# Optimization experiments

Hardware: AMD Instinct MI355X
Metric: run time of the kernel (lower is better)

The kernel has to match this reference:

```python
import jax, jax.numpy as jnp
import numpy as np

LN_EPS = 1e-5

def setup_inputs() -> dict:
    key = jax.random.key(0)
    k1, k2, k3 = jax.random.split(key, 3)
    L, B, D = 2048, 8, 1024
    x = jax.random.normal(k1, (L, B, D), dtype=jnp.float32)
    c = jnp.zeros((B, D), dtype=jnp.float32)
    W = jax.random.normal(k2, (D, 3 * D), dtype=jnp.float32) * 0.02
    # bias init from _init_bias: u-bias 0, f-bias 0.5, r-bias 0
    b = jnp.concatenate([jnp.zeros(D), jnp.full((D,), 0.5), jnp.zeros(D)]).astype(jnp.float32)
    gamma = jnp.ones((D,), dtype=jnp.float32)
    beta = jnp.zeros((D,), dtype=jnp.float32)
    return {"x": x, "c": c, "W": W, "b": b, "gamma": gamma, "beta": beta}

def reference(x, c, W, b, gamma, beta):
    # LayerNorm over last dim
    mu = jnp.mean(x, axis=-1, keepdims=True)
    var = jnp.mean(jnp.square(x - mu), axis=-1, keepdims=True)
    x_norm = (x - mu) * jax.lax.rsqrt(var + LN_EPS) * gamma + beta
    # Fused u/f/r projection: [L,B,3D]
    ufr = jnp.einsum('lbd,de->lbe', x_norm, W) + b
    u, f, r = jnp.split(ufr, 3, axis=-1)
    f_gate = jax.nn.sigmoid(f)
    r_gate = jax.nn.sigmoid(r)
    # Linear recurrence c_t = f_t * c_{t-1} + (1-f_t) * u_t via scan over time
    def step(c_prev, fu):
        f_t, u_t = fu
        c_t = f_t * c_prev + (1.0 - f_t) * u_t
        return c_t, c_t
    last_c, c_stack = jax.lax.scan(step, c, (f_gate, u))
    hs = r_gate * jnp.tanh(c_stack) + (1.0 - r_gate) * x_norm
    return x + hs, last_c
```

## Files before the change

kernel.cpp:

```cpp
#include <hip/hip_runtime.h>
#include <hip/hip_bf16.h>


typedef unsigned short u16;
typedef __bf16 bf16x8 __attribute__((ext_vector_type(8)));
typedef float f32x4 __attribute__((ext_vector_type(4)));

#define L_DIM 2048
#define B_DIM 8
#define D_DIM 1024
#define M_DIM (L_DIM * B_DIM)
#define K_DIM D_DIM
#define N_DIM (3 * D_DIM)
#define NCH 32
#define CLEN (L_DIM / NCH)
#define NT (K_DIM / 64)

#define LDS_A 0
#define LDS_B 65536
#define LDS_DUMMY 131072
#define LDS_TOTAL 147456

__device__ __forceinline__ float bf2f(u16 h) {
    unsigned int u = ((unsigned int)h) << 16;
    float f;
    __builtin_memcpy(&f, &u, 4);
    return f;
}

__device__ __forceinline__ u16 f2bf(float f) {
    unsigned int u;
    __builtin_memcpy(&u, &f, 4);
    u = u + 0x7fff + ((u >> 16) & 1);
    return (u16)(u >> 16);
}

__device__ __forceinline__ void async16(void* lds, const void* g) {
    __builtin_amdgcn_global_load_lds(
        (const __attribute__((address_space(1))) void*)g,
        (__attribute__((address_space(3))) void*)lds, 16, 0, 0);
}

__global__ __launch_bounds__(256) void ln_kernel(const float* __restrict__ x,
                                                 const float* __restrict__ gamma,
                                                 const float* __restrict__ beta,
                                                 u16* __restrict__ xn) {
    int row = blockIdx.x;
    int tid = threadIdx.x;
    const float4* xr = (const float4*)(x + (size_t)row * D_DIM);
    float4 v = xr[tid];
    float s = v.x + v.y + v.z + v.w;
    float q = v.x * v.x + v.y * v.y + v.z * v.z + v.w * v.w;
    #pragma unroll
    for (int off = 32; off; off >>= 1) {
        s += __shfl_down(s, off);
        q += __shfl_down(q, off);
    }
    __shared__ float ss[4], qq[4];
    int lane = tid & 63, wv = tid >> 6;
    if (lane == 0) { ss[wv] = s; qq[wv] = q; }
    __syncthreads();
    s = ss[0] + ss[1] + ss[2] + ss[3];
    q = qq[0] + qq[1] + qq[2] + qq[3];
    float mu = s * (1.0f / D_DIM);
    float var = q * (1.0f / D_DIM) - mu * mu;
    float rs = rsqrtf(var + 1e-5f);
    float4 g = ((const float4*)gamma)[tid];
    float4 bt = ((const float4*)beta)[tid];
    ushort4 o;
    o.x = f2bf((v.x - mu) * rs * g.x + bt.x);
    o.y = f2bf((v.y - mu) * rs * g.y + bt.y);
    o.z = f2bf((v.z - mu) * rs * g.z + bt.z);
    o.w = f2bf((v.w - mu) * rs * g.w + bt.w);
    ((ushort4*)(xn + (size_t)row * D_DIM))[tid] = o;
}

__global__ __launch_bounds__(256) void wt_kernel(const float* __restrict__ W,
                                                 u16* __restrict__ Wt) {
    __shared__ float t[64][65];
    int k0 = blockIdx.x * 64;
    int n0 = blockIdx.y * 64;
    int col = threadIdx.x & 63;
    int rg4 = threadIdx.x >> 6;
    #pragma unroll
    for (int j = 0; j < 16; ++j) {
        int r = rg4 * 16 + j;
        t[r][col] = W[(size_t)(k0 + r) * N_DIM + n0 + col];
    }
    __syncthreads();
    #pragma unroll
    for (int j = 0; j < 16; ++j) {
        int nr = rg4 * 16 + j;
        Wt[(size_t)(n0 + nr) * K_DIM + k0 + col] = f2bf(t[col][nr]);
    }
}

__device__ __forceinline__ void stage_half(const u16* __restrict__ gsrc, int base0,
                                           int t, int h, char* lds, int ldsOp,
                                           int tid, int wave) {
    int tc = (t < NT) ? t : 0;
    int k0 = tc * 64;
    char* dst0 = (t < NT) ? (lds + ldsOp + (t & 1) * 32768 + h * 16384)
                          : (lds + LDS_DUMMY);
    #pragma unroll
    for (int s = 0; s < 2; ++s) {
        int c = s * 512 + tid;
        int row = h * 128 + (c >> 3);
        int cc = (c & 7) ^ (row & 7);
        async16(dst0 + s * 8192 + wave * 1024,
                gsrc + (size_t)(base0 + row) * K_DIM + k0 + cc * 8);
    }
}

__global__ __launch_bounds__(512, 2) void gemm_kernel(const u16* __restrict__ A,
                                                      const u16* __restrict__ Bt,
                                                      const float* __restrict__ bias,
                                                      u16* __restrict__ uo,
                                                      u16* __restrict__ fo,
                                                      u16* __restrict__ ro) {
    extern __shared__ char lds[];
    const int tid = threadIdx.x;
    const int wave = tid >> 6, lane = tid & 63;
    const int lm = lane & 15, lg = lane >> 4;
    const int wm = wave >> 2, wn = wave & 3;
    const int m0 = blockIdx.x * 256;
    const int n0 = blockIdx.y * 256;

    f32x4 acc[8][4] = {};
    bf16x8 av[4][2], aw[4][2], bv[4][2];

#define LDA(dst, bb, mf0)                                                       \
    do { _Pragma("unroll")                                                      \
        for (int q = 0; q < 4; ++q) {                                           \
            int row_ = wm * 128 + ((mf0) + q) * 16 + lm;                        \
            const char* p_ = lds + LDS_A + (bb) * 32768 + row_ * 128;           \
            _Pragma("unroll")                                                   \
            for (int kk = 0; kk < 2; ++kk)                                      \
                dst[q][kk] = *(const bf16x8*)(p_ + ((((kk << 2) | lg) ^ (row_ & 7)) << 4)); \
        } } while (0)

#define LDB(bb, kk)                                                             \
    do { _Pragma("unroll")                                                      \
        for (int nf = 0; nf < 4; ++nf) {                                        \
            int row_ = wn * 64 + nf * 16 + lm;                                  \
            bv[nf][kk] = *(const bf16x8*)(lds + LDS_B + (bb) * 32768 + row_ * 128 \
                                          + ((((kk << 2) | lg) ^ (row_ & 7)) << 4)); \
        } } while (0)

#define MFMA16(r0, afr, kk)                                                     \
    do { _Pragma("unroll")                                                      \
        for (int q = 0; q < 4; ++q)                                             \
            _Pragma("unroll")                                                   \
            for (int nf = 0; nf < 4; ++nf)                                      \
                acc[(r0) + q][nf] = __builtin_amdgcn_mfma_f32_16x16x32_bf16(    \
                    afr[q][kk], bv[nf][kk], acc[(r0) + q][nf], 0, 0, 0);        \
    } while (0)

#define PH_SYNC()                                                               \
    do { __builtin_amdgcn_s_barrier();                                          \
         asm volatile("s_waitcnt lgkmcnt(0)");                                  \
         __builtin_amdgcn_sched_barrier(0); } while (0)

#define TILE_BODY(t, bb, last)                                                  \
    do {                                                                        \
                 \
        LDA(av, bb, 0);                                                         \
        LDB(bb, 0);                                                             \
        stage_half(A, m0, (t) + 1, 0, lds, LDS_A, tid, wave);                   \
        PH_SYNC();                                                              \
        __builtin_amdgcn_s_setprio(1);                                          \
        MFMA16(0, av, 0);                                                       \
        __builtin_amdgcn_s_setprio(0);                                          \
        __builtin_amdgcn_s_barrier();                                           \
                                     \
        LDB(bb, 1);                                                             \
        stage_half(A, m0, (t) + 1, 1, lds, LDS_A, tid, wave);                   \
        PH_SYNC();                                                              \
        __builtin_amdgcn_s_setprio(1);                                          \
        MFMA16(0, av, 1);                                                       \
        __builtin_amdgcn_s_setprio(0);                                          \
        __builtin_amdgcn_s_barrier();                                           \
                                   \
        LDA(aw, bb, 4);                                                         \
        stage_half(Bt, n0, (t) + 2, 0, lds, LDS_B, tid, wave);                  \
        PH_SYNC();                                                              \
        __builtin_amdgcn_s_setprio(1);                                          \
        MFMA16(4, aw, 0);                                                       \
        __builtin_amdgcn_s_setprio(0);                                          \
        __builtin_amdgcn_s_barrier();                                           \
                         \
        stage_half(Bt, n0, (t) + 2, 1, lds, LDS_B, tid, wave);                  \
        __builtin_amdgcn_s_barrier();                                           \
        __builtin_amdgcn_s_setprio(1);                                          \
        MFMA16(4, aw, 1);                                                       \
        __builtin_amdgcn_s_setprio(0);                                          \
        if (!(last)) asm volatile("s_waitcnt vmcnt(4)" ::: "memory");           \
        __builtin_amdgcn_s_barrier();                                           \
    } while (0)

    stage_half(A, m0, 0, 0, lds, LDS_A, tid, wave);
    stage_half(A, m0, 0, 1, lds, LDS_A, tid, wave);
    stage_half(Bt, n0, 0, 0, lds, LDS_B, tid, wave);
    stage_half(Bt, n0, 0, 1, lds, LDS_B, tid, wave);
    stage_half(Bt, n0, 1, 0, lds, LDS_B, tid, wave);
    stage_half(Bt, n0, 1, 1, lds, LDS_B, tid, wave);
    asm volatile("s_waitcnt vmcnt(4)" ::: "memory");
    __builtin_amdgcn_s_barrier();

    for (int t = 0; t < NT - 2; t += 2) {
        TILE_BODY(t, 0, 0);
        TILE_BODY(t + 1, 1, 0);
    }
    TILE_BODY(NT - 2, 0, 0);
    TILE_BODY(NT - 1, 1, 1);

    int seg = n0 >> 10;
    u16* outp = (seg == 0) ? uo : ((seg == 1) ? fo : ro);
    #pragma unroll
    for (int mf = 0; mf < 8; ++mf) {
        #pragma unroll
        for (int nf = 0; nf < 4; ++nf) {
            int col = n0 + wn * 64 + nf * 16 + lm;
            int cm = col & 1023;
            float bb2 = bias[col];
            #pragma unroll
            for (int j = 0; j < 4; ++j) {
                int row = m0 + wm * 128 + mf * 16 + lg * 4 + j;
                float val = acc[mf][nf][j] + bb2;
                if (seg != 0) val = 1.0f / (1.0f + __expf(-val));
                outp[(size_t)row * D_DIM + cm] = f2bf(val);
            }
        }
    }
#undef LDA
#undef LDB
#undef MFMA16
#undef PH_SYNC
#undef TILE_BODY
}

__global__ __launch_bounds__(256) void scan1_kernel(const u16* __restrict__ fg,
                                                    const u16* __restrict__ u,
                                                    float* __restrict__ Aa,
                                                    float* __restrict__ Ss) {
    int ch = blockIdx.x;
    int bd = (blockIdx.y * 256 + threadIdx.x) * 2;
    int b = bd >> 10, d = bd & 1023;
    float a0 = 1.0f, a1 = 1.0f, s0 = 0.0f, s1 = 0.0f;
    for (int t = ch * CLEN; t < ch * CLEN + CLEN; ++t) {
        size_t idx = ((size_t)(t * B_DIM + b) << 10) + d;
        ushort2 f2 = *(const ushort2*)(fg + idx);
        ushort2 u2 = *(const ushort2*)(u + idx);
        float f0 = bf2f(f2.x), f1 = bf2f(f2.y);
        float v0 = bf2f(u2.x), v1 = bf2f(u2.y);
        s0 = f0 * s0 + (1.0f - f0) * v0;
        s1 = f1 * s1 + (1.0f - f1) * v1;
        a0 *= f0;
        a1 *= f1;
    }
    int o = ch * 8192 + bd;
    *(float2*)(Aa + o) = make_float2(a0, a1);
    *(float2*)(Ss + o) = make_float2(s0, s1);
}

__global__ __launch_bounds__(256) void scan2_kernel(const float* __restrict__ Aa,
                                                    const float* __restrict__ Ss,
                                                    const float* __restrict__ c0,
                                                    float* __restrict__ cs,
                                                    float* __restrict__ lastc) {
    int bd = blockIdx.x * 256 + threadIdx.x;
    float c = c0[bd];
    #pragma unroll 4
    for (int ch = 0; ch < NCH; ++ch) {
        cs[ch * 8192 + bd] = c;
        c = Aa[ch * 8192 + bd] * c + Ss[ch * 8192 + bd];
    }
    lastc[bd] = c;
}

__global__ __launch_bounds__(256) void scan3_kernel(const float* __restrict__ cs,
                                                    const u16* __restrict__ fg,
                                                    const u16* __restrict__ u,
                                                    const u16* __restrict__ rg,
                                                    const u16* __restrict__ xn,
                                                    const float* __restrict__ x,
                                                    float* __restrict__ out) {
    int ch = blockIdx.x;
    int bd = (blockIdx.y * 256 + threadIdx.x) * 2;
    int b = bd >> 10, d = bd & 1023;
    float c0v = cs[ch * 8192 + bd];
    float c1v = cs[ch * 8192 + bd + 1];
    for (int t = ch * CLEN; t < ch * CLEN + CLEN; ++t) {
        size_t idx = ((size_t)(t * B_DIM + b) << 10) + d;
        ushort2 f2 = *(const ushort2*)(fg + idx);
        ushort2 u2 = *(const ushort2*)(u + idx);
        ushort2 r2 = *(const ushort2*)(rg + idx);
        ushort2 n2 = *(const ushort2*)(xn + idx);
        float2 x2 = *(const float2*)(x + idx);
        float f0 = bf2f(f2.x), f1 = bf2f(f2.y);
        float v0 = bf2f(u2.x), v1 = bf2f(u2.y);
        float r0 = bf2f(r2.x), r1 = bf2f(r2.y);
        float n0 = bf2f(n2.x), n1 = bf2f(n2.y);
        c0v = f0 * c0v + (1.0f - f0) * v0;
        c1v = f1 * c1v + (1.0f - f1) * v1;
        float h0 = r0 * tanhf(c0v) + (1.0f - r0) * n0;
        float h1 = r1 * tanhf(c1v) + (1.0f - r1) * n1;
        *(float2*)(out + idx) = make_float2(x2.x + h0, x2.y + h1);
    }
}

extern "C" void kernel_launch(void* const* d_in, const int* in_sizes, int n_in,
                              void* d_out, int out_size, void* d_ws, size_t ws_size,
                              hipStream_t stream) {
    const float* x     = (const float*)d_in[0];
    const float* c0    = (const float*)d_in[1];
    const float* W     = (const float*)d_in[2];
    const float* b     = (const float*)d_in[3];
    const float* gamma = (const float*)d_in[4];
    const float* beta  = (const float*)d_in[5];
    float* out = (float*)d_out;
    float* lastc = out + (size_t)M_DIM * D_DIM;

    char* w = (char*)d_ws;
    u16* xn = (u16*)w;  w += (size_t)M_DIM * D_DIM * 2;
    u16* Wt = (u16*)w;  w += (size_t)N_DIM * K_DIM * 2;
    u16* ug = (u16*)w;  w += (size_t)M_DIM * D_DIM * 2;
    u16* fg = (u16*)w;  w += (size_t)M_DIM * D_DIM * 2;
    u16* rg = (u16*)w;  w += (size_t)M_DIM * D_DIM * 2;
    float* Aa = (float*)w; w += (size_t)NCH * 8192 * 4;
    float* Ss = (float*)w; w += (size_t)NCH * 8192 * 4;
    float* cs = (float*)w; w += (size_t)NCH * 8192 * 4;

    hipFuncSetAttribute(reinterpret_cast<const void*>(gemm_kernel),
                        hipFuncAttributeMaxDynamicSharedMemorySize, LDS_TOTAL);

    ln_kernel<<<M_DIM, 256, 0, stream>>>(x, gamma, beta, xn);
    wt_kernel<<<dim3(K_DIM / 64, N_DIM / 64), 256, 0, stream>>>(W, Wt);
    gemm_kernel<<<dim3(M_DIM / 256, N_DIM / 256), 512, LDS_TOTAL, stream>>>(xn, Wt, b, ug, fg, rg);
    scan1_kernel<<<dim3(NCH, 16), 256, 0, stream>>>(fg, ug, Aa, Ss);
    scan2_kernel<<<32, 256, 0, stream>>>(Aa, Ss, c0, cs, lastc);
    scan3_kernel<<<dim3(NCH, 16), 256, 0, stream>>>(cs, fg, ug, rg, xn, x, out);
}
```

Baseline: 215.8 us.

## Remap GEMM blocks across XCDs, reorder staging, recompute x_norm in final scan

The GEMM grid becomes 1D with a block-index remap that places consecutive tiles on the same XCD (bid&7 stride) to improve L2 reuse. Global-to-LDS staging is issued before the LDS fragment reads in each phase, and the epilogue loop order is swapped so the bias is loaded once per column. The final scan kernel stops reading the bf16 xn buffer and instead recomputes x_norm from x using per-row mean and rstd saved by the LN kernel plus gamma and beta, which removes a 32MB read and uses fp32 x_norm instead of bf16 in the residual. The remap and the staging reorder could change the GEMM's cache behaviour and scheduling in either direction.

```diff
diff --git a/kernel.cpp b/kernel.cpp
--- a/kernel.cpp
+++ b/kernel.cpp
@@ -44,7 +44,8 @@
 __global__ __launch_bounds__(256) void ln_kernel(const float* __restrict__ x,
                                                  const float* __restrict__ gamma,
                                                  const float* __restrict__ beta,
-                                                 u16* __restrict__ xn) {
+                                                 u16* __restrict__ xn,
+                                                 float2* __restrict__ mrs) {
     int row = blockIdx.x;
     int tid = threadIdx.x;
     const float4* xr = (const float4*)(x + (size_t)row * D_DIM);
@@ -65,6 +66,7 @@
     float mu = s * (1.0f / D_DIM);
     float var = q * (1.0f / D_DIM) - mu * mu;
     float rs = rsqrtf(var + 1e-5f);
+    if (tid == 0) mrs[row] = make_float2(mu, rs);
     float4 g = ((const float4*)gamma)[tid];
     float4 bt = ((const float4*)beta)[tid];
     ushort4 o;
@@ -123,8 +125,10 @@
     const int wave = tid >> 6, lane = tid & 63;
     const int lm = lane & 15, lg = lane >> 4;
     const int wm = wave >> 2, wn = wave & 3;
-    const int m0 = blockIdx.x * 256;
-    const int n0 = blockIdx.y * 256;
+    const int bid = blockIdx.x;
+    const int wg = (bid & 7) * 96 + (bid >> 3);
+    const int m0 = (wg & 63) * 256;
+    const int n0 = (wg >> 6) * 256;
 
     f32x4 acc[8][4] = {};
     bf16x8 av[4][2], aw[4][2], bv[4][2];
@@ -163,36 +167,29 @@
 
 #define TILE_BODY(t, bb, last)                                                  \
     do {                                                                        \
-                 \
+             \
+        stage_half(A, m0, (t) + 1, 0, lds, LDS_A, tid, wave);                   \
         LDA(av, bb, 0);                                                         \
         LDB(bb, 0);                                                             \
-        stage_half(A, m0, (t) + 1, 0, lds, LDS_A, tid, wave);                   \
         PH_SYNC();                                                              \
-        __builtin_amdgcn_s_setprio(1);                                          \
-        MFMA16(0, av, 0);                                                       \
-        __builtin_amdgcn_s_setprio(0);                                          \
-        __builtin_amdgcn_s_barrier();                                           \
-                                     \
+        __builtin_amdgcn_s_setprio(1);  MFMA16(0, av, 0);                       \
+        __builtin_amdgcn_s_setprio(0);  __builtin_amdgcn_s_barrier();           \
+                                  \
+        stage_half(A, m0, (t) + 1, 1, lds, LDS_A, tid, wave);                   \
         LDB(bb, 1);                                                             \
-        stage_half(A, m0, (t) + 1, 1, lds, LDS_A, tid, wave);                   \
         PH_SYNC();                                                              \
-        __builtin_amdgcn_s_setprio(1);                                          \
-        MFMA16(0, av, 1);                                                       \
-        __builtin_amdgcn_s_setprio(0);                                          \
-        __builtin_amdgcn_s_barrier();                                           \
+        __builtin_amdgcn_s_setprio(1);  MFMA16(0, av, 1);                       \
+        __builtin_amdgcn_s_setprio(0);  __builtin_amdgcn_s_barrier();           \
+                                \
+        stage_half(Bt, n0, (t) + 2, 0, lds, LDS_B, tid, wave);                  \
+        LDA(aw, bb, 4);                                                         \
+        PH_SYNC();                                                              \
+        __builtin_amdgcn_s_setprio(1);  MFMA16(4, aw, 0);                       \
+        __builtin_amdgcn_s_setprio(0);  __builtin_amdgcn_s_barrier();           \
                                    \
-        LDA(aw, bb, 4);                                                         \
-        stage_half(Bt, n0, (t) + 2, 0, lds, LDS_B, tid, wave);                  \
-        PH_SYNC();                                                              \
-        __builtin_amdgcn_s_setprio(1);                                          \
-        MFMA16(4, aw, 0);                                                       \
-        __builtin_amdgcn_s_setprio(0);                                          \
-        __builtin_amdgcn_s_barrier();                                           \
-                         \
         stage_half(Bt, n0, (t) + 2, 1, lds, LDS_B, tid, wave);                  \
         __builtin_amdgcn_s_barrier();                                           \
-        __builtin_amdgcn_s_setprio(1);                                          \
-        MFMA16(4, aw, 1);                                                       \
+        __builtin_amdgcn_s_setprio(1);  MFMA16(4, aw, 1);                       \
         __builtin_amdgcn_s_setprio(0);                                          \
         if (!(last)) asm volatile("s_waitcnt vmcnt(4)" ::: "memory");           \
         __builtin_amdgcn_s_barrier();                                           \
@@ -217,12 +214,12 @@
     int seg = n0 >> 10;
     u16* outp = (seg == 0) ? uo : ((seg == 1) ? fo : ro);
     #pragma unroll
-    for (int mf = 0; mf < 8; ++mf) {
+    for (int nf = 0; nf < 4; ++nf) {
+        int col = n0 + wn * 64 + nf * 16 + lm;
+        int cm = col & 1023;
+        float bb2 = bias[col];
         #pragma unroll
-        for (int nf = 0; nf < 4; ++nf) {
-            int col = n0 + wn * 64 + nf * 16 + lm;
-            int cm = col & 1023;
-            float bb2 = bias[col];
+        for (int mf = 0; mf < 8; ++mf) {
             #pragma unroll
             for (int j = 0; j < 4; ++j) {
                 int row = m0 + wm * 128 + mf * 16 + lg * 4 + j;
@@ -282,12 +279,16 @@
                                                     const u16* __restrict__ fg,
                                                     const u16* __restrict__ u,
                                                     const u16* __restrict__ rg,
-                                                    const u16* __restrict__ xn,
+                                                    const float2* __restrict__ mrs,
+                                                    const float* __restrict__ gamma,
+                                                    const float* __restrict__ beta,
                                                     const float* __restrict__ x,
                                                     float* __restrict__ out) {
     int ch = blockIdx.x;
     int bd = (blockIdx.y * 256 + threadIdx.x) * 2;
     int b = bd >> 10, d = bd & 1023;
+    float2 gm = *(const float2*)(gamma + d);
+    float2 bt = *(const float2*)(beta + d);
     float c0v = cs[ch * 8192 + bd];
     float c1v = cs[ch * 8192 + bd + 1];
     for (int t = ch * CLEN; t < ch * CLEN + CLEN; ++t) {
@@ -295,12 +296,13 @@
         ushort2 f2 = *(const ushort2*)(fg + idx);
         ushort2 u2 = *(const ushort2*)(u + idx);
         ushort2 r2 = *(const ushort2*)(rg + idx);
-        ushort2 n2 = *(const ushort2*)(xn + idx);
         float2 x2 = *(const float2*)(x + idx);
+        float2 mr = mrs[t * B_DIM + b];
         float f0 = bf2f(f2.x), f1 = bf2f(f2.y);
         float v0 = bf2f(u2.x), v1 = bf2f(u2.y);
         float r0 = bf2f(r2.x), r1 = bf2f(r2.y);
-        float n0 = bf2f(n2.x), n1 = bf2f(n2.y);
+        float n0 = (x2.x - mr.x) * mr.y * gm.x + bt.x;
+        float n1 = (x2.y - mr.x) * mr.y * gm.y + bt.y;
         c0v = f0 * c0v + (1.0f - f0) * v0;
         c1v = f1 * c1v + (1.0f - f1) * v1;
         float h0 = r0 * tanhf(c0v) + (1.0f - r0) * n0;
@@ -330,14 +332,15 @@
     float* Aa = (float*)w; w += (size_t)NCH * 8192 * 4;
     float* Ss = (float*)w; w += (size_t)NCH * 8192 * 4;
     float* cs = (float*)w; w += (size_t)NCH * 8192 * 4;
+    float2* mrs = (float2*)w; w += (size_t)M_DIM * 8;
 
     hipFuncSetAttribute(reinterpret_cast<const void*>(gemm_kernel),
                         hipFuncAttributeMaxDynamicSharedMemorySize, LDS_TOTAL);
 
-    ln_kernel<<<M_DIM, 256, 0, stream>>>(x, gamma, beta, xn);
+    ln_kernel<<<M_DIM, 256, 0, stream>>>(x, gamma, beta, xn, mrs);
     wt_kernel<<<dim3(K_DIM / 64, N_DIM / 64), 256, 0, stream>>>(W, Wt);
-    gemm_kernel<<<dim3(M_DIM / 256, N_DIM / 256), 512, LDS_TOTAL, stream>>>(xn, Wt, b, ug, fg, rg);
+    gemm_kernel<<<768, 512, LDS_TOTAL, stream>>>(xn, Wt, b, ug, fg, rg);
     scan1_kernel<<<dim3(NCH, 16), 256, 0, stream>>>(fg, ug, Aa, Ss);
     scan2_kernel<<<32, 256, 0, stream>>>(Aa, Ss, c0, cs, lastc);
-    scan3_kernel<<<dim3(NCH, 16), 256, 0, stream>>>(cs, fg, ug, rg, xn, x, out);
-}
+    scan3_kernel<<<dim3(NCH, 16), 256, 0, stream>>>(cs, fg, ug, rg, mrs, gamma, beta, x, out);
+}
```

After: 237.2 us. 1.1x slower.
